# Kernel optimization log

Measured on AMD Instinct MI355X. Metric: run time of the kernel, lower is better.

## Reference

```python
import math
import jax
import jax.numpy as jnp
import numpy as np

N_QUBITS = 4
N_LAYERS = 2


def _ry(t):
    # t: [] or [B] real angle -> [2,2] or [B,2,2] complex RY matrix
    c, s = jnp.cos(t * 0.5), jnp.sin(t * 0.5)
    return jnp.stack([jnp.stack([c, -s], -1), jnp.stack([s, c], -1)], -2).astype(jnp.complex64)


def _rz(t):
    # t: [] or [B] real angle -> diag(e^{-it/2}, e^{+it/2}) complex RZ matrix
    ph = jnp.exp(-0.5j * t.astype(jnp.complex64))
    z = jnp.zeros_like(ph)
    return jnp.stack([jnp.stack([ph, z], -1), jnp.stack([z, jnp.conj(ph)], -1)], -2)


def _apply_1q(psi, U, w):
    # psi: [B,2,2,2,2]; U: [2,2] (shared) or [B,2,2] (per-sample); wire w
    psi = jnp.moveaxis(psi, 1 + w, -1)
    if U.ndim == 3:
        out = jnp.einsum('bij,bpqrj->bpqri', U, psi)
    else:
        out = jnp.einsum('ij,bpqrj->bpqri', U, psi)
    return jnp.moveaxis(out, -1, 1 + w)


def _cnot(psi, c):
    # CNOT with control wire c, target wire c+1 (matches qml.CNOT([w, w+1]))
    a0 = jax.lax.index_in_dim(psi, 0, axis=1 + c, keepdims=False)
    a1 = jax.lax.index_in_dim(psi, 1, axis=1 + c, keepdims=False)
    a1 = jnp.flip(a1, axis=1 + c)
    return jnp.stack([a0, a1], axis=1 + c)


def _circuit(angles, q_weights):
    # angles: [B,4] real; q_weights: [n_layers,4,2]
    B = angles.shape[0]
    psi = jnp.zeros((B, 2, 2, 2, 2), jnp.complex64).at[:, 0, 0, 0, 0].set(1.0)
    for layer in range(N_LAYERS):
        for w in range(N_QUBITS):
            psi = _apply_1q(psi, _ry(angles[:, w]), w)
            psi = _apply_1q(psi, _rz((layer + 1) * angles[:, w]), w)
        for w in range(N_QUBITS):
            psi = _apply_1q(psi, _ry(q_weights[layer, w, 0]), w)
            psi = _apply_1q(psi, _rz(q_weights[layer, w, 1]), w)
        for w in range(N_QUBITS - 1):
            psi = _cnot(psi, w)
    p = psi.real ** 2 + psi.imag ** 2  # [B,2,2,2,2] probabilities
    zs = []
    for w in range(N_QUBITS):
        axes = tuple(a for a in range(1, 1 + N_QUBITS) if a != 1 + w)
        s = jnp.sum(p, axis=axes)  # [B,2]
        zs.append(s[:, 0] - s[:, 1])
    return jnp.stack(zs, -1).astype(jnp.float32)  # [B,4] <Z_w> expvals


def setup_inputs() -> dict:
    key = jax.random.key(0)
    ks = jax.random.split(key, 8)
    B, D = 131072, 256
    return {
        'x': jax.random.normal(ks[0], (B, D), jnp.float32),
        'w_proj': jax.random.normal(ks[1], (4, D), jnp.float32) / np.float32(np.sqrt(D)),
        'b_proj': jnp.zeros((4,), jnp.float32),
        'q_weights': 0.01 * jax.random.normal(ks[2], (2, 4, 2), jnp.float32),
        'w_h': jax.random.normal(ks[3], (16, 4), jnp.float32) * np.float32(0.5),
        'b_h': jnp.zeros((16,), jnp.float32),
        'w_out': jax.random.normal(ks[4], (10, 16), jnp.float32) * np.float32(0.25),
        'b_out': jnp.zeros((10,), jnp.float32),
    }


def reference(x, w_proj, b_proj, q_weights, w_h, b_h, w_out, b_out):
    # input_proj -> tanh * pi -> per-sample quantum circuit -> MLP classifier
    angles = jnp.tanh(x @ w_proj.T + b_proj) * np.float32(math.pi)  # [B,4]
    q = _circuit(angles, q_weights)                                  # [B,4]
    h = jax.nn.relu(q @ w_h.T + b_h)                                 # [B,16]
    return h @ w_out.T + b_out                                       # [B,10]
```

## Files before the change

### kernel.cpp

```cpp
#include <hip/hip_runtime.h>
#include <math.h>

#define D    256
#define BLK  64
#define CH   32
#define NCH  (D/CH)

struct C2 { float x, y; };

__device__ __forceinline__ void gate_ry(C2 st[16], const int m, float c, float s) {
#pragma unroll
  for (int i = 0; i < 16; ++i) {
    if (i & m) continue;
    const int i1 = i | m;
    C2 a0 = st[i], a1 = st[i1];
    st[i].x  = c*a0.x - s*a1.x;  st[i].y  = c*a0.y - s*a1.y;
    st[i1].x = s*a0.x + c*a1.x;  st[i1].y = s*a0.y + c*a1.y;
  }
}

__device__ __forceinline__ void gate_rz(C2 st[16], const int m, float c, float s) {
#pragma unroll
  for (int i = 0; i < 16; ++i) {
    C2 a = st[i];
    if (i & m) { st[i].x = a.x*c - a.y*s; st[i].y = a.y*c + a.x*s; }
    else       { st[i].x = a.x*c + a.y*s; st[i].y = a.y*c - a.x*s; }
  }
}

__global__ __launch_bounds__(BLK, 4) void qhead_kernel(
    const float4* __restrict__ x4,
    const float*  __restrict__ w_proj,
    const float*  __restrict__ b_proj,
    const float*  __restrict__ qw,
    const float*  __restrict__ w_h,
    const float*  __restrict__ b_h,
    const float*  __restrict__ w_out,
    const float*  __restrict__ b_out,
    float*        __restrict__ out)
{
  __shared__ float4 wpT[D];
  __shared__ float  xt[CH][BLK + 1];

  const int tid = threadIdx.x;
  const long s0 = (long)blockIdx.x * BLK;
  const long xbase = s0 * (D / 4);

#pragma unroll
  for (int r = 0; r < 4; ++r) {
    const int k = r * BLK + tid;
    wpT[k] = make_float4(w_proj[k], w_proj[D + k], w_proj[2*D + k], w_proj[3*D + k]);
  }

  float4 v[8];
#pragma unroll
  for (int i = 0; i < 8; ++i) {
    const int s = i * 8 + (tid >> 3), k4 = tid & 7;
    v[i] = x4[xbase + (long)s * (D/4) + k4];
  }
  float4 acc = make_float4(0.f, 0.f, 0.f, 0.f);
#pragma unroll 1
  for (int c = 0; c < NCH; ++c) {
    __syncthreads();
#pragma unroll
    for (int i = 0; i < 8; ++i) {
      const int s  = i * 8 + (tid >> 3);
      const int kk = (tid & 7) * 4;
      xt[kk + 0][s] = v[i].x; xt[kk + 1][s] = v[i].y;
      xt[kk + 2][s] = v[i].z; xt[kk + 3][s] = v[i].w;
    }
    __syncthreads();
    if (c + 1 < NCH) {
#pragma unroll
      for (int i = 0; i < 8; ++i) {
        const int s = i * 8 + (tid >> 3), k4 = tid & 7;
        v[i] = x4[xbase + (long)s * (D/4) + (c + 1) * 8 + k4];
      }
    }
#pragma unroll 8
    for (int k = 0; k < CH; ++k) {
      const float  xv = xt[k][tid];
      const float4 w  = wpT[c * CH + k];
      acc.x += xv * w.x; acc.y += xv * w.y; acc.z += xv * w.z; acc.w += xv * w.w;
    }
  }

  const float PI_F = 3.14159265358979f;
  float ang[4];
  ang[0] = tanhf(acc.x + b_proj[0]) * PI_F;
  ang[1] = tanhf(acc.y + b_proj[1]) * PI_F;
  ang[2] = tanhf(acc.z + b_proj[2]) * PI_F;
  ang[3] = tanhf(acc.w + b_proj[3]) * PI_F;

  float ch[4], sh[4], cf[4], sf[4];
#pragma unroll
  for (int w = 0; w < 4; ++w) {
    __sincosf(0.5f * ang[w], &sh[w], &ch[w]);
    __sincosf(ang[w], &sf[w], &cf[w]);
  }

  C2 st[16];
#pragma unroll
  for (int i = 0; i < 16; ++i) { st[i].x = 0.f; st[i].y = 0.f; }
  st[0].x = 1.f;

#pragma unroll
  for (int layer = 0; layer < 2; ++layer) {
#pragma unroll
    for (int w = 0; w < 4; ++w) {
      gate_ry(st, 8 >> w, ch[w], sh[w]);
      if (layer == 0) gate_rz(st, 8 >> w, ch[w], sh[w]);
      else            gate_rz(st, 8 >> w, cf[w], sf[w]);
    }
#pragma unroll
    for (int w = 0; w < 4; ++w) {
      float cw, sw, cz, sz;
      __sincosf(0.5f * qw[(layer * 4 + w) * 2 + 0], &sw, &cw);
      __sincosf(0.5f * qw[(layer * 4 + w) * 2 + 1], &sz, &cz);
      gate_ry(st, 8 >> w, cw, sw);
      gate_rz(st, 8 >> w, cz, sz);
    }
#pragma unroll
    for (int w = 0; w < 3; ++w) {
      const int mc = 8 >> w, mt = 4 >> w;
#pragma unroll
      for (int i = 0; i < 16; ++i) {
        if ((i & mc) && !(i & mt)) {
          C2 t2 = st[i]; st[i] = st[i | mt]; st[i | mt] = t2;
        }
      }
    }
  }

  float z[4] = {0.f, 0.f, 0.f, 0.f};
#pragma unroll
  for (int i = 0; i < 16; ++i) {
    const float p = st[i].x * st[i].x + st[i].y * st[i].y;
#pragma unroll
    for (int w = 0; w < 4; ++w) z[w] += (i & (8 >> w)) ? -p : p;
  }

  float outv[10];
  {
    float h[16];
#pragma unroll
    for (int j = 0; j < 16; ++j) {
      float a = b_h[j];
#pragma unroll
      for (int w = 0; w < 4; ++w) a += w_h[j * 4 + w] * z[w];
      h[j] = fmaxf(a, 0.f);
    }
#pragma unroll
    for (int o = 0; o < 10; ++o) {
      float a = b_out[o];
#pragma unroll
      for (int j = 0; j < 16; ++j) a += w_out[o * 16 + j] * h[j];
      outv[o] = a;
    }
  }

  __syncthreads();
  float* outS = &xt[0][0];
#pragma unroll
  for (int o = 0; o < 10; ++o) outS[tid * 11 + o] = outv[o];
  __syncthreads();
  float* og = out + (long)blockIdx.x * (BLK * 10);
#pragma unroll
  for (int i = 0; i < 10; ++i) {
    const int j = i * BLK + tid;
    og[j] = outS[(j / 10) * 11 + (j % 10)];
  }
}

extern "C" void kernel_launch(void* const* d_in, const int* in_sizes, int n_in,
                              void* d_out, int out_size, void* d_ws, size_t ws_size,
                              hipStream_t stream) {
  const int B = in_sizes[0] / D;
  dim3 grid(B / BLK), block(BLK);
  qhead_kernel<<<grid, block, 0, stream>>>(
      (const float4*)d_in[0],
      (const float*)d_in[1], (const float*)d_in[2], (const float*)d_in[3],
      (const float*)d_in[4], (const float*)d_in[5], (const float*)d_in[6],
      (const float*)d_in[7], (float*)d_out);
}
```

Before: 210.7 us.

## Replace LDS transpose projection with row-contiguous loads and shuffle butterfly reduction

The input projection changes thread mapping. Each lane now owns four contiguous columns of every row, so each 8-row chunk is a fully contiguous 1 KB-per-row read. Per-row partial dot products are combined with a xor-shuffle butterfly that reduces and transposes at once, leaving each lane with one sample's projected features. This removes the shared-memory transpose tile, the per-chunk barriers and the shared weight staging, at the cost of many cross-lane shuffles (ds_bpermute on AMD). The output staging is remapped to the new sample-to-lane assignment.

```diff
diff --git a/kernel.cpp b/kernel.cpp
--- a/kernel.cpp
+++ b/kernel.cpp
@@ -3,10 +3,20 @@
 
 #define D    256
 #define BLK  64
-#define CH   32
-#define NCH  (D/CH)
+#define RPC  8
+#define NCH  (BLK/RPC)
 
 struct C2 { float x, y; };
+
+__device__ __forceinline__ float4 shfl_xor4(float4 a, int m) {
+  float4 r;
+  r.x = __shfl_xor(a.x, m); r.y = __shfl_xor(a.y, m);
+  r.z = __shfl_xor(a.z, m); r.w = __shfl_xor(a.w, m);
+  return r;
+}
+__device__ __forceinline__ float4 add4(float4 a, float4 b) {
+  return make_float4(a.x+b.x, a.y+b.y, a.z+b.z, a.w+b.w);
+}
 
 __device__ __forceinline__ void gate_ry(C2 st[16], const int m, float c, float s) {
 #pragma unroll
@@ -39,50 +49,66 @@
     const float*  __restrict__ b_out,
     float*        __restrict__ out)
 {
-  __shared__ float4 wpT[D];
-  __shared__ float  xt[CH][BLK + 1];
+  __shared__ float outS[BLK * 11];
 
   const int tid = threadIdx.x;
   const long s0 = (long)blockIdx.x * BLK;
-  const long xbase = s0 * (D / 4);
-
-#pragma unroll
-  for (int r = 0; r < 4; ++r) {
-    const int k = r * BLK + tid;
-    wpT[k] = make_float4(w_proj[k], w_proj[D + k], w_proj[2*D + k], w_proj[3*D + k]);
-  }
+  const float4* xrow = x4 + s0 * (D / 4);
+
+  float4 wj[4];
+#pragma unroll
+  for (int j = 0; j < 4; ++j)
+    wj[j] = *(const float4*)(w_proj + j * D + 4 * tid);
 
   float4 v[8];
 #pragma unroll
-  for (int i = 0; i < 8; ++i) {
-    const int s = i * 8 + (tid >> 3), k4 = tid & 7;
-    v[i] = x4[xbase + (long)s * (D/4) + k4];
-  }
+  for (int i = 0; i < 8; ++i) v[i] = xrow[(long)i * (D/4) + tid];
+
+  const int b5 = (tid >> 5) & 1, b4 = (tid >> 4) & 1, b3 = (tid >> 3) & 1;
+  const int csel = tid & 7;
   float4 acc = make_float4(0.f, 0.f, 0.f, 0.f);
+
 #pragma unroll 1
   for (int c = 0; c < NCH; ++c) {
-    __syncthreads();
+    float4 p[8];
 #pragma unroll
     for (int i = 0; i < 8; ++i) {
-      const int s  = i * 8 + (tid >> 3);
-      const int kk = (tid & 7) * 4;
-      xt[kk + 0][s] = v[i].x; xt[kk + 1][s] = v[i].y;
-      xt[kk + 2][s] = v[i].z; xt[kk + 3][s] = v[i].w;
-    }
-    __syncthreads();
+      p[i].x = v[i].x*wj[0].x + v[i].y*wj[0].y + v[i].z*wj[0].z + v[i].w*wj[0].w;
+      p[i].y = v[i].x*wj[1].x + v[i].y*wj[1].y + v[i].z*wj[1].z + v[i].w*wj[1].w;
+      p[i].z = v[i].x*wj[2].x + v[i].y*wj[2].y + v[i].z*wj[2].z + v[i].w*wj[2].w;
+      p[i].w = v[i].x*wj[3].x + v[i].y*wj[3].y + v[i].z*wj[3].z + v[i].w*wj[3].w;
+    }
     if (c + 1 < NCH) {
 #pragma unroll
-      for (int i = 0; i < 8; ++i) {
-        const int s = i * 8 + (tid >> 3), k4 = tid & 7;
-        v[i] = x4[xbase + (long)s * (D/4) + (c + 1) * 8 + k4];
-      }
-    }
-#pragma unroll 8
-    for (int k = 0; k < CH; ++k) {
-      const float  xv = xt[k][tid];
-      const float4 w  = wpT[c * CH + k];
-      acc.x += xv * w.x; acc.y += xv * w.y; acc.z += xv * w.z; acc.w += xv * w.w;
-    }
+      for (int i = 0; i < 8; ++i)
+        v[i] = xrow[((long)(c + 1) * RPC + i) * (D/4) + tid];
+    }
+    float4 q[4];
+#pragma unroll
+    for (int i = 0; i < 4; ++i) {
+      float4 send = b5 ? p[i] : p[i + 4];
+      float4 keep = b5 ? p[i + 4] : p[i];
+      q[i] = add4(keep, shfl_xor4(send, 32));
+    }
+    float4 u[2];
+#pragma unroll
+    for (int i = 0; i < 2; ++i) {
+      float4 send = b4 ? u[0] : u[0];
+      (void)send;
+      float4 s2 = b4 ? q[i] : q[i + 2];
+      float4 k2 = b4 ? q[i + 2] : q[i];
+      u[i] = add4(k2, shfl_xor4(s2, 16));
+    }
+    float4 t;
+    {
+      float4 s3 = b3 ? u[0] : u[1];
+      float4 k3 = b3 ? u[1] : u[0];
+      t = add4(k3, shfl_xor4(s3, 8));
+    }
+    t = add4(t, shfl_xor4(t, 4));
+    t = add4(t, shfl_xor4(t, 2));
+    t = add4(t, shfl_xor4(t, 1));
+    if (csel == c) acc = t;
   }
 
   const float PI_F = 3.14159265358979f;
@@ -159,10 +185,9 @@
     }
   }
 
-  __syncthreads();
-  float* outS = &xt[0][0];
-#pragma unroll
-  for (int o = 0; o < 10; ++o) outS[tid * 11 + o] = outv[o];
+  const int smp = 8 * csel + (tid >> 3);
+#pragma unroll
+  for (int o = 0; o < 10; ++o) outS[smp * 11 + o] = outv[o];
   __syncthreads();
   float* og = out + (long)blockIdx.x * (BLK * 10);
 #pragma unroll
```

Result: no change. 210.8 us (+0.1%).
